# Kernel optimization log

Hardware: AMD Instinct MI355X
Metric: run time of the kernel (lower is better)

## Reference

```python
import jax, jax.numpy as jnp
import numpy as np

AGENT_RADIUS = 0.5
SAFETY_DIST = 0.1
QP_ITERS = 300


def _qp_solve(p, G, h):
    """Batched QP: min_u 0.5 u^T u + p^T u  s.t.  G u <= h  (Q = I).
    Solved in the dual by projected gradient ascent (differentiable, fixed iters).
    p: [B,2], G: [B,m,2], h: [B,m] -> u: [B,2]
    """
    GGt = jnp.einsum('bmi,bni->bmn', G, G)                 # [B,m,m]
    q = jnp.einsum('bmi,bi->bm', G, p) + h                 # [B,m]
    # Lipschitz upper bound per sample (Frobenius norm of GG^T)
    L = jnp.sqrt(jnp.sum(GGt * GGt, axis=(1, 2))) + 1e-6   # [B]
    alpha = (1.0 / L)[:, None]

    def step(lam, _):
        grad = jnp.einsum('bmn,bn->bm', GGt, lam) + q
        lam = jnp.maximum(lam - alpha * grad, 0.0)
        return lam, None

    lam0 = jnp.zeros_like(h)
    lam, _ = jax.lax.scan(step, lam0, None, length=QP_ITERS)
    u = -p - jnp.einsum('bmi,bm->bi', G, lam)
    return u


def setup_inputs() -> dict:
    key = jax.random.key(0)
    ks = jax.random.split(key, 20)
    B, F, H1, H2 = 8192, 8, 1024, 512

    def w(k, i, o):
        return (jax.random.normal(k, (i, o), jnp.float32) / np.sqrt(i)).astype(jnp.float32)

    obs_xy = jax.random.uniform(ks[17], (8, 2), jnp.float32, -10.0, 10.0)
    obs_r = jax.random.uniform(ks[18], (8, 1), jnp.float32, 0.3, 0.8)
    return {
        'x': jax.random.normal(ks[0], (B, F), jnp.float32),
        'mean': 0.1 * jax.random.normal(ks[1], (F,), jnp.float32),
        'std': jax.random.uniform(ks[2], (F,), jnp.float32, 0.5, 1.5),
        'W1': w(ks[3], F, H1), 'b1': jnp.zeros((H1,), jnp.float32),
        'W21': w(ks[4], H1, H2), 'b21': jnp.zeros((H2,), jnp.float32),
        'W22': w(ks[5], H1, H2), 'b22': jnp.zeros((H2,), jnp.float32),
        'W23': w(ks[6], H1, H2), 'b23': jnp.zeros((H2,), jnp.float32),
        'W31': w(ks[7], H2, 2), 'b31': jnp.zeros((2,), jnp.float32),
        'W32': w(ks[8], H2, 2), 'b32': jnp.zeros((2,), jnp.float32),
        'W33': w(ks[9], H2, 1), 'b33': jnp.zeros((1,), jnp.float32),
        'obstacles': jnp.concatenate([obs_xy, obs_r], axis=1),  # [8,3] (x,y,r)
        'sgn': 1,
    }


def reference(x, mean, std, W1, b1, W21, b21, W22, b22, W23, b23,
              W31, b31, W32, b32, W33, b33, obstacles, sgn):
    B = x.shape[0]
    x0 = x * std + mean                                   # un-normalized state [B,8]

    h1 = jax.nn.relu(x @ W1 + b1)
    x21 = jax.nn.relu(h1 @ W21 + b21)
    x22 = jax.nn.relu(h1 @ W22 + b22)
    x23 = jax.nn.relu(h1 @ W23 + b23)
    x31 = x21 @ W31 + b31                                 # QP linear term p [B,2]
    x32 = 4.0 * jax.nn.sigmoid(x22 @ W32 + b32)           # CBF gains p1,p2 [B,2]
    x33 = 4.0 * jax.nn.sigmoid(x23 @ W33 + b33)           # liveness gain (unused, smg off)

    px, py, theta, v = x0[:, 0], x0[:, 1], x0[:, 2], x0[:, 3]
    st, ct = jnp.sin(theta)[:, None], jnp.cos(theta)[:, None]
    vb = v[:, None]

    # static obstacles broadcast to batch + opponent as last obstacle -> [B, m]
    ox = jnp.concatenate([jnp.broadcast_to(obstacles[:, 0][None], (B, obstacles.shape[0])), x0[:, 4:5]], axis=1)
    oy = jnp.concatenate([jnp.broadcast_to(obstacles[:, 1][None], (B, obstacles.shape[0])), x0[:, 5:6]], axis=1)
    orad = jnp.concatenate([jnp.broadcast_to(obstacles[:, 2][None], (B, obstacles.shape[0])),
                            jnp.full((B, 1), AGENT_RADIUS, x0.dtype)], axis=1)

    R = AGENT_RADIUS + orad + SAFETY_DIST
    dx = px[:, None] - ox                                  # [B,m]
    dy = py[:, None] - oy

    barrier = dx * dx + dy * dy - R * R
    barrier_dot = 2.0 * dx * vb * ct + 2.0 * dy * vb * st
    Lf2b = (2.0 * v * v)[:, None]
    LgLfbu1 = -2.0 * dx * vb * st + 2.0 * dy * vb * ct
    LgLfbu2 = 2.0 * dx * ct + 2.0 * dy * st
    G = jnp.stack([-LgLfbu1, -LgLfbu2], axis=-1)           # [B,m,2]
    p1, p2 = x32[:, 0:1], x32[:, 1:2]
    h = Lf2b + (p1 + p2) * barrier_dot + p1 * p2 * barrier # [B,m]

    u = _qp_solve(x31, G, h)                               # [B,2]
    return u
```

## Files before the change

### kernel.cpp

```cpp
#include <hip/hip_runtime.h>
#include <cstdint>
#include <cstddef>

typedef unsigned short u16;
typedef u16   u16x8  __attribute__((ext_vector_type(8)));
typedef u16   u16x4  __attribute__((ext_vector_type(4)));
typedef __bf16 bf16x8 __attribute__((ext_vector_type(8)));
typedef float f32x4  __attribute__((ext_vector_type(4)));
typedef float f32x2  __attribute__((ext_vector_type(2)));

__device__ __forceinline__ float bf2f(u16 v) {
  unsigned int u = ((unsigned int)v) << 16;
  return __builtin_bit_cast(float, u);
}
__device__ __forceinline__ u16 f2bf(float f) {
  unsigned int x = __builtin_bit_cast(unsigned int, f);
  x += 0x7fffu + ((x >> 16) & 1u);
  return (u16)(x >> 16);
}

__global__ __launch_bounds__(256) void k_prep(const float* __restrict__ W21,
                                              const float* __restrict__ W22,
                                              u16* __restrict__ Wt,
                                              const float* __restrict__ x,
                                              const float* __restrict__ W1,
                                              const float* __restrict__ b1,
                                              u16* __restrict__ h1,
                                              float* __restrict__ head) {
  __shared__ u16 s[64][65];
  const int b = blockIdx.x;
  if (b < 256) {
    const int mat = b >> 7;
    const int tt  = b & 127;
    const int k0  = (tt >> 3) * 64;
    const int n0  = (tt & 7) * 64;
    const float* W = mat ? W22 : W21;
    const int tx = threadIdx.x & 63;
    const int ty = threadIdx.x >> 6;
#pragma unroll
    for (int i = 0; i < 16; ++i) {
      int r = i * 4 + ty;
      s[r][tx] = f2bf(W[(size_t)(k0 + r) * 512 + n0 + tx]);
    }
    __syncthreads();
    const int nbase = mat * 512 + n0;
#pragma unroll
    for (int i = 0; i < 16; ++i) {
      int r = i * 4 + ty;
      Wt[(size_t)(nbase + r) * 1024 + k0 + tx] = s[tx][r];
    }
  } else {
    const int row = b - 256;
    if (threadIdx.x == 0)
      *(f32x4*)(head + 4 * (size_t)row) = f32x4{0.f, 0.f, 0.f, 0.f};
    const int c4 = threadIdx.x * 4;
    const float* xr = x + (size_t)row * 8;
    f32x4 acc = *(const f32x4*)(b1 + c4);
#pragma unroll
    for (int f = 0; f < 8; ++f) {
      float xv = xr[f];
      f32x4 wv = *(const f32x4*)(W1 + f * 1024 + c4);
#pragma unroll
      for (int e = 0; e < 4; ++e) acc[e] = fmaf(xv, wv[e], acc[e]);
    }
    u16x4 o;
#pragma unroll
    for (int e = 0; e < 4; ++e) o[e] = f2bf(fmaxf(acc[e], 0.f));
    *(u16x4*)(h1 + (size_t)row * 1024 + c4) = o;
  }
}

__global__ __launch_bounds__(256) void k_gemm(const u16* __restrict__ A,
                                              const u16* __restrict__ Bt,
                                              const float* __restrict__ b21,
                                              const float* __restrict__ b22,
                                              const float* __restrict__ W31,
                                              const float* __restrict__ W32,
                                              float* __restrict__ head) {
  constexpr int K  = 1024;
  constexpr int BK = 32;
  constexpr int NT = K / BK;
  __shared__ u16 As[2][128 * BK];
  __shared__ u16 Bs[2][128 * BK];

  const int t    = threadIdx.x;
  const int row0 = blockIdx.y * 128;
  const int col0 = blockIdx.x * 128;
  const int w    = t >> 6;
  const int lane = t & 63;
  const int wr   = w >> 1, wc = w & 1;
  const int lrow = lane & 15;
  const int lk   = (lane >> 4) * 8;

  const int c0 = t, c1 = 256 + t;
  const u16* gA0 = A  + (size_t)(row0 + (c0 >> 2)) * K + (c0 & 3) * 8;
  const u16* gA1 = A  + (size_t)(row0 + (c1 >> 2)) * K + (c1 & 3) * 8;
  const u16* gB0 = Bt + (size_t)(col0 + (c0 >> 2)) * K + (c0 & 3) * 8;
  const u16* gB1 = Bt + (size_t)(col0 + (c1 >> 2)) * K + (c1 & 3) * 8;
  const int lo0 = c0 * 8, lo1 = c1 * 8;

  f32x4 acc[4][4];
#pragma unroll
  for (int i = 0; i < 4; ++i)
#pragma unroll
    for (int j = 0; j < 4; ++j) acc[i][j] = f32x4{0.f, 0.f, 0.f, 0.f};

  {
    u16x8 ta0 = *(const u16x8*)gA0;
    u16x8 ta1 = *(const u16x8*)gA1;
    u16x8 tb0 = *(const u16x8*)gB0;
    u16x8 tb1 = *(const u16x8*)gB1;
    *(u16x8*)(As[0] + lo0) = ta0;
    *(u16x8*)(As[0] + lo1) = ta1;
    *(u16x8*)(Bs[0] + lo0) = tb0;
    *(u16x8*)(Bs[0] + lo1) = tb1;
  }
  u16x8 na0 = *(const u16x8*)(gA0 + BK);
  u16x8 na1 = *(const u16x8*)(gA1 + BK);
  u16x8 nb0 = *(const u16x8*)(gB0 + BK);
  u16x8 nb1 = *(const u16x8*)(gB1 + BK);

  for (int kt = 0; kt < NT; ++kt) {
    const int cur = kt & 1, nxt = cur ^ 1;
    __syncthreads();

    const int koff = (kt + 2 < NT ? kt + 2 : NT - 1) * BK;
    u16x8 fa0 = *(const u16x8*)(gA0 + koff);
    u16x8 fa1 = *(const u16x8*)(gA1 + koff);
    u16x8 fb0 = *(const u16x8*)(gB0 + koff);
    u16x8 fb1 = *(const u16x8*)(gB1 + koff);

    bf16x8 af[4], bfr[4];
#pragma unroll
    for (int i = 0; i < 4; ++i)
      af[i] = __builtin_bit_cast(bf16x8,
          *(const u16x8*)(As[cur] + (wr * 64 + i * 16 + lrow) * BK + lk));
#pragma unroll
    for (int j = 0; j < 4; ++j)
      bfr[j] = __builtin_bit_cast(bf16x8,
          *(const u16x8*)(Bs[cur] + (wc * 64 + j * 16 + lrow) * BK + lk));
#pragma unroll
    for (int i = 0; i < 4; ++i)
#pragma unroll
      for (int j = 0; j < 4; ++j)
        acc[i][j] = __builtin_amdgcn_mfma_f32_16x16x32_bf16(af[i], bfr[j], acc[i][j], 0, 0, 0);

    if (kt + 1 < NT) {
      *(u16x8*)(As[nxt] + lo0) = na0;
      *(u16x8*)(As[nxt] + lo1) = na1;
      *(u16x8*)(Bs[nxt] + lo0) = nb0;
      *(u16x8*)(Bs[nxt] + lo1) = nb1;
    }
    na0 = fa0; na1 = fa1; nb0 = fb0; nb1 = fb1;
  }

  const bool isX21 = (col0 < 512);
  const float* Wh  = isX21 ? W31 : W32;
  const int   hoff = isX21 ? 0 : 2;

  float hx[16], hy[16];
#pragma unroll
  for (int n = 0; n < 16; ++n) { hx[n] = 0.f; hy[n] = 0.f; }
#pragma unroll
  for (int j = 0; j < 4; ++j) {
    int col  = col0 + wc * 64 + j * 16 + lrow;
    int wcol = col & 511;
    f32x2 wv = *(const f32x2*)(Wh + 2 * wcol);
    float bias = isX21 ? b21[col] : b22[wcol];
#pragma unroll
    for (int i = 0; i < 4; ++i)
#pragma unroll
      for (int rr = 0; rr < 4; ++rr) {
        float v = fmaxf(acc[i][j][rr] + bias, 0.f);
        hx[i * 4 + rr] = fmaf(v, wv[0], hx[i * 4 + rr]);
        hy[i * 4 + rr] = fmaf(v, wv[1], hy[i * 4 + rr]);
      }
  }
#pragma unroll
  for (int m = 1; m <= 8; m <<= 1) {
#pragma unroll
    for (int n = 0; n < 16; ++n) {
      hx[n] += __shfl_xor(hx[n], m, 64);
      hy[n] += __shfl_xor(hy[n], m, 64);
    }
  }
  if (lrow == 0) {
    const int rq = (lane >> 4) * 4;
#pragma unroll
    for (int i = 0; i < 4; ++i)
#pragma unroll
      for (int rr = 0; rr < 4; ++rr) {
        int row = row0 + wr * 64 + i * 16 + rq + rr;
        atomicAdd(head + 4 * (size_t)row + hoff,     hx[i * 4 + rr]);
        atomicAdd(head + 4 * (size_t)row + hoff + 1, hy[i * 4 + rr]);
      }
  }
}

__global__ __launch_bounds__(256) void k_qp(const float* __restrict__ x,
                                            const float* __restrict__ mean_,
                                            const float* __restrict__ std_,
                                            const float* __restrict__ head,
                                            const float* __restrict__ b31,
                                            const float* __restrict__ b32,
                                            const float* __restrict__ obstacles,
                                            float* __restrict__ out) {
  const int r = blockIdx.x * 256 + threadIdx.x;
  f32x4 hd = *(const f32x4*)(head + 4 * (size_t)r);
  float p0  = hd[0] + b31[0];
  float p1v = hd[1] + b31[1];
  float pp1 = 4.f / (1.f + expf(-(hd[2] + b32[0])));
  float pp2 = 4.f / (1.f + expf(-(hd[3] + b32[1])));

  const f32x4* xp = (const f32x4*)(x + (size_t)r * 8);
  f32x4 xa = xp[0], xb = xp[1];
  float px = xa[0] * std_[0] + mean_[0];
  float py = xa[1] * std_[1] + mean_[1];
  float th = xa[2] * std_[2] + mean_[2];
  float v  = xa[3] * std_[3] + mean_[3];
  float ax = xb[0] * std_[4] + mean_[4];
  float ay = xb[1] * std_[5] + mean_[5];
  float st = sinf(th), ct = cosf(th);
  float Lf2b = 2.f * v * v;

  float G0[9], G1[9], q[9];
  float s00 = 0.f, s01 = 0.f, s11 = 0.f;
#pragma unroll
  for (int m = 0; m < 9; ++m) {
    float ox, oy, orad;
    if (m < 8) {
      ox = obstacles[m * 3]; oy = obstacles[m * 3 + 1]; orad = obstacles[m * 3 + 2];
    } else { ox = ax; oy = ay; orad = 0.5f; }
    float R  = 0.6f + orad;
    float dx = px - ox, dy = py - oy;
    float bar  = dx * dx + dy * dy - R * R;
    float dct  = dx * ct + dy * st;
    float bdot = 2.f * v * dct;
    float g0 = 2.f * v * (dx * st - dy * ct);
    float g1 = -2.f * dct;
    float h  = Lf2b + (pp1 + pp2) * bdot + pp1 * pp2 * bar;
    G0[m] = g0; G1[m] = g1;
    q[m] = g0 * p0 + g1 * p1v + h;
    s00 += g0 * g0; s01 += g0 * g1; s11 += g1 * g1;
  }
  float L = sqrtf(s00 * s00 + 2.f * s01 * s01 + s11 * s11) + 1e-6f;
  float alpha = 1.f / L;

  float lam[9];
#pragma unroll
  for (int m = 0; m < 9; ++m) lam[m] = 0.f;
  for (int it = 0; it < 300; ++it) {
    float pr0[9], pr1[9];
#pragma unroll
    for (int m = 0; m < 9; ++m) { pr0[m] = G0[m] * lam[m]; pr1[m] = G1[m] * lam[m]; }
    float t0 = (((pr0[0] + pr0[1]) + (pr0[2] + pr0[3])) +
                ((pr0[4] + pr0[5]) + (pr0[6] + pr0[7]))) + pr0[8];
    float t1 = (((pr1[0] + pr1[1]) + (pr1[2] + pr1[3])) +
                ((pr1[4] + pr1[5]) + (pr1[6] + pr1[7]))) + pr1[8];
#pragma unroll
    for (int m = 0; m < 9; ++m) {
      float g = fmaf(G0[m], t0, fmaf(G1[m], t1, q[m]));
      lam[m] = fmaxf(fmaf(-alpha, g, lam[m]), 0.f);
    }
  }
  float u0 = -p0, u1 = -p1v;
#pragma unroll
  for (int m = 0; m < 9; ++m) { u0 = fmaf(-G0[m], lam[m], u0); u1 = fmaf(-G1[m], lam[m], u1); }
  *(f32x2*)(out + 2 * (size_t)r) = f32x2{u0, u1};
}

extern "C" void kernel_launch(void* const* d_in, const int* in_sizes, int n_in,
                              void* d_out, int out_size, void* d_ws, size_t ws_size,
                              hipStream_t stream) {
  const float* x    = (const float*)d_in[0];
  const float* mean_= (const float*)d_in[1];
  const float* std_ = (const float*)d_in[2];
  const float* W1   = (const float*)d_in[3];
  const float* b1   = (const float*)d_in[4];
  const float* W21  = (const float*)d_in[5];
  const float* b21  = (const float*)d_in[6];
  const float* W22  = (const float*)d_in[7];
  const float* b22  = (const float*)d_in[8];
  const float* W31  = (const float*)d_in[11];
  const float* b31  = (const float*)d_in[12];
  const float* W32  = (const float*)d_in[13];
  const float* b32  = (const float*)d_in[14];
  const float* obst = (const float*)d_in[17];
  float* out = (float*)d_out;

  char* ws = (char*)d_ws;
  u16*   Wt   = (u16*)ws;
  u16*   h1   = (u16*)(ws + (size_t)(1 << 21));
  float* head = (float*)(ws + (size_t)(1 << 21) + (size_t)(1 << 24));

  k_prep<<<256 + 8192, 256, 0, stream>>>(W21, W22, Wt, x, W1, b1, h1, head);
  k_gemm<<<dim3(8, 64), 256, 0, stream>>>(h1, Wt, b21, b22, W31, W32, head);
  k_qp  <<<32, 256, 0, stream>>>(x, mean_, std_, head, b31, b32, obst, out);
}
```

Before: 171.6 us.

## Retile head GEMM to 64x64 blocks with 32x32 MFMA and padded LDS

```diff
diff --git a/kernel.cpp b/kernel.cpp
--- a/kernel.cpp
+++ b/kernel.cpp
@@ -8,6 +8,7 @@
 typedef __bf16 bf16x8 __attribute__((ext_vector_type(8)));
 typedef float f32x4  __attribute__((ext_vector_type(4)));
 typedef float f32x2  __attribute__((ext_vector_type(2)));
+typedef float f32x16 __attribute__((ext_vector_type(16)));
 
 __device__ __forceinline__ float bf2f(u16 v) {
   unsigned int u = ((unsigned int)v) << 16;
@@ -50,27 +51,35 @@
       Wt[(size_t)(nbase + r) * 1024 + k0 + tx] = s[tx][r];
     }
   } else {
-    const int row = b - 256;
-    if (threadIdx.x == 0)
-      *(f32x4*)(head + 4 * (size_t)row) = f32x4{0.f, 0.f, 0.f, 0.f};
+    const int row0 = (b - 256) * 8;
+    if (threadIdx.x < 8)
+      *(f32x4*)(head + 4 * (size_t)(row0 + threadIdx.x)) = f32x4{0.f, 0.f, 0.f, 0.f};
     const int c4 = threadIdx.x * 4;
-    const float* xr = x + (size_t)row * 8;
-    f32x4 acc = *(const f32x4*)(b1 + c4);
+    f32x4 bv = *(const f32x4*)(b1 + c4);
+    f32x4 acc[8];
+#pragma unroll
+    for (int r = 0; r < 8; ++r) acc[r] = bv;
 #pragma unroll
     for (int f = 0; f < 8; ++f) {
-      float xv = xr[f];
       f32x4 wv = *(const f32x4*)(W1 + f * 1024 + c4);
 #pragma unroll
-      for (int e = 0; e < 4; ++e) acc[e] = fmaf(xv, wv[e], acc[e]);
-    }
-    u16x4 o;
-#pragma unroll
-    for (int e = 0; e < 4; ++e) o[e] = f2bf(fmaxf(acc[e], 0.f));
-    *(u16x4*)(h1 + (size_t)row * 1024 + c4) = o;
-  }
-}
-
-__global__ __launch_bounds__(256) void k_gemm(const u16* __restrict__ A,
+      for (int r = 0; r < 8; ++r) {
+        float xv = x[(size_t)(row0 + r) * 8 + f];
+#pragma unroll
+        for (int e = 0; e < 4; ++e) acc[r][e] = fmaf(xv, wv[e], acc[r][e]);
+      }
+    }
+#pragma unroll
+    for (int r = 0; r < 8; ++r) {
+      u16x4 o;
+#pragma unroll
+      for (int e = 0; e < 4; ++e) o[e] = f2bf(fmaxf(acc[r][e], 0.f));
+      *(u16x4*)(h1 + (size_t)(row0 + r) * 1024 + c4) = o;
+    }
+  }
+}
+
+__global__ __launch_bounds__(128) void k_gemm(const u16* __restrict__ A,
                                               const u16* __restrict__ Bt,
                                               const float* __restrict__ b21,
                                               const float* __restrict__ b22,
@@ -80,120 +89,97 @@
   constexpr int K  = 1024;
   constexpr int BK = 32;
   constexpr int NT = K / BK;
-  __shared__ u16 As[2][128 * BK];
-  __shared__ u16 Bs[2][128 * BK];
+  constexpr int ST = 40;
+  __shared__ u16 As[64 * ST];
+  __shared__ u16 Bs[64 * ST];
 
   const int t    = threadIdx.x;
-  const int row0 = blockIdx.y * 128;
-  const int col0 = blockIdx.x * 128;
+  const int col0 = blockIdx.x * 64;
+  const int row0 = blockIdx.y * 64;
   const int w    = t >> 6;
   const int lane = t & 63;
-  const int wr   = w >> 1, wc = w & 1;
-  const int lrow = lane & 15;
-  const int lk   = (lane >> 4) * 8;
-
-  const int c0 = t, c1 = 256 + t;
+  const int ln   = lane & 31;
+  const int kh   = lane >> 5;
+
+  const int c0 = t, c1 = 128 + t;
   const u16* gA0 = A  + (size_t)(row0 + (c0 >> 2)) * K + (c0 & 3) * 8;
   const u16* gA1 = A  + (size_t)(row0 + (c1 >> 2)) * K + (c1 & 3) * 8;
   const u16* gB0 = Bt + (size_t)(col0 + (c0 >> 2)) * K + (c0 & 3) * 8;
   const u16* gB1 = Bt + (size_t)(col0 + (c1 >> 2)) * K + (c1 & 3) * 8;
-  const int lo0 = c0 * 8, lo1 = c1 * 8;
-
-  f32x4 acc[4][4];
-#pragma unroll
-  for (int i = 0; i < 4; ++i)
-#pragma unroll
-    for (int j = 0; j < 4; ++j) acc[i][j] = f32x4{0.f, 0.f, 0.f, 0.f};
-
-  {
-    u16x8 ta0 = *(const u16x8*)gA0;
-    u16x8 ta1 = *(const u16x8*)gA1;
-    u16x8 tb0 = *(const u16x8*)gB0;
-    u16x8 tb1 = *(const u16x8*)gB1;
-    *(u16x8*)(As[0] + lo0) = ta0;
-    *(u16x8*)(As[0] + lo1) = ta1;
-    *(u16x8*)(Bs[0] + lo0) = tb0;
-    *(u16x8*)(Bs[0] + lo1) = tb1;
-  }
-  u16x8 na0 = *(const u16x8*)(gA0 + BK);
-  u16x8 na1 = *(const u16x8*)(gA1 + BK);
-  u16x8 nb0 = *(const u16x8*)(gB0 + BK);
-  u16x8 nb1 = *(const u16x8*)(gB1 + BK);
+  const int lA0 = (c0 >> 2) * ST + (c0 & 3) * 8;
+  const int lA1 = (c1 >> 2) * ST + (c1 & 3) * 8;
+
+  f32x16 acc0, acc1;
+#pragma unroll
+  for (int e = 0; e < 16; ++e) { acc0[e] = 0.f; acc1[e] = 0.f; }
+
+  u16x8 ra0 = *(const u16x8*)gA0;
+  u16x8 ra1 = *(const u16x8*)gA1;
+  u16x8 rb0 = *(const u16x8*)gB0;
+  u16x8 rb1 = *(const u16x8*)gB1;
 
   for (int kt = 0; kt < NT; ++kt) {
-    const int cur = kt & 1, nxt = cur ^ 1;
     __syncthreads();
-
-    const int koff = (kt + 2 < NT ? kt + 2 : NT - 1) * BK;
-    u16x8 fa0 = *(const u16x8*)(gA0 + koff);
-    u16x8 fa1 = *(const u16x8*)(gA1 + koff);
-    u16x8 fb0 = *(const u16x8*)(gB0 + koff);
-    u16x8 fb1 = *(const u16x8*)(gB1 + koff);
-
-    bf16x8 af[4], bfr[4];
-#pragma unroll
-    for (int i = 0; i < 4; ++i)
-      af[i] = __builtin_bit_cast(bf16x8,
-          *(const u16x8*)(As[cur] + (wr * 64 + i * 16 + lrow) * BK + lk));
-#pragma unroll
-    for (int j = 0; j < 4; ++j)
-      bfr[j] = __builtin_bit_cast(bf16x8,
-          *(const u16x8*)(Bs[cur] + (wc * 64 + j * 16 + lrow) * BK + lk));
-#pragma unroll
-    for (int i = 0; i < 4; ++i)
-#pragma unroll
-      for (int j = 0; j < 4; ++j)
-        acc[i][j] = __builtin_amdgcn_mfma_f32_16x16x32_bf16(af[i], bfr[j], acc[i][j], 0, 0, 0);
-
+    *(u16x8*)(As + lA0) = ra0;
+    *(u16x8*)(As + lA1) = ra1;
+    *(u16x8*)(Bs + lA0) = rb0;
+    *(u16x8*)(Bs + lA1) = rb1;
     if (kt + 1 < NT) {
-      *(u16x8*)(As[nxt] + lo0) = na0;
-      *(u16x8*)(As[nxt] + lo1) = na1;
-      *(u16x8*)(Bs[nxt] + lo0) = nb0;
-      *(u16x8*)(Bs[nxt] + lo1) = nb1;
-    }
-    na0 = fa0; na1 = fa1; nb0 = fb0; nb1 = fb1;
-  }
-
-  const bool isX21 = (col0 < 512);
-  const float* Wh  = isX21 ? W31 : W32;
-  const int   hoff = isX21 ? 0 : 2;
-
-  float hx[16], hy[16];
-#pragma unroll
-  for (int n = 0; n < 16; ++n) { hx[n] = 0.f; hy[n] = 0.f; }
-#pragma unroll
-  for (int j = 0; j < 4; ++j) {
-    int col  = col0 + wc * 64 + j * 16 + lrow;
-    int wcol = col & 511;
-    f32x2 wv = *(const f32x2*)(Wh + 2 * wcol);
-    float bias = isX21 ? b21[col] : b22[wcol];
-#pragma unroll
-    for (int i = 0; i < 4; ++i)
-#pragma unroll
-      for (int rr = 0; rr < 4; ++rr) {
-        float v = fmaxf(acc[i][j][rr] + bias, 0.f);
-        hx[i * 4 + rr] = fmaf(v, wv[0], hx[i * 4 + rr]);
-        hy[i * 4 + rr] = fmaf(v, wv[1], hy[i * 4 + rr]);
+      const int ko = (kt + 1) * BK;
+      ra0 = *(const u16x8*)(gA0 + ko);
+      ra1 = *(const u16x8*)(gA1 + ko);
+      rb0 = *(const u16x8*)(gB0 + ko);
+      rb1 = *(const u16x8*)(gB1 + ko);
+    }
+    __syncthreads();
+
+    bf16x8 a0s0 = __builtin_bit_cast(bf16x8, *(const u16x8*)(As + (ln)      * ST +      kh * 8));
+    bf16x8 a1s0 = __builtin_bit_cast(bf16x8, *(const u16x8*)(As + (32 + ln) * ST +      kh * 8));
+    bf16x8 b_s0 = __builtin_bit_cast(bf16x8, *(const u16x8*)(Bs + (w * 32 + ln) * ST +  kh * 8));
+    bf16x8 a0s1 = __builtin_bit_cast(bf16x8, *(const u16x8*)(As + (ln)      * ST + 16 + kh * 8));
+    bf16x8 a1s1 = __builtin_bit_cast(bf16x8, *(const u16x8*)(As + (32 + ln) * ST + 16 + kh * 8));
+    bf16x8 b_s1 = __builtin_bit_cast(bf16x8, *(const u16x8*)(Bs + (w * 32 + ln) * ST + 16 + kh * 8));
+
+    acc0 = __builtin_amdgcn_mfma_f32_32x32x16_bf16(a0s0, b_s0, acc0, 0, 0, 0);
+    acc1 = __builtin_amdgcn_mfma_f32_32x32x16_bf16(a1s0, b_s0, acc1, 0, 0, 0);
+    acc0 = __builtin_amdgcn_mfma_f32_32x32x16_bf16(a0s1, b_s1, acc0, 0, 0, 0);
+    acc1 = __builtin_amdgcn_mfma_f32_32x32x16_bf16(a1s1, b_s1, acc1, 0, 0, 0);
+  }
+
+  const int col   = col0 + w * 32 + ln;
+  const bool isX21 = (col < 512);
+  const float* Wh = isX21 ? W31 : W32;
+  const int  hoff = isX21 ? 0 : 2;
+  const int  wcol = col & 511;
+  f32x2 wv = *(const f32x2*)(Wh + 2 * wcol);
+  const float bias = isX21 ? b21[col] : b22[wcol];
+
+#pragma unroll
+  for (int i = 0; i < 2; ++i) {
+    f32x16 a = i ? acc1 : acc0;
+    float hx[16], hy[16];
+#pragma unroll
+    for (int r = 0; r < 16; ++r) {
+      float v = fmaxf(a[r] + bias, 0.f);
+      hx[r] = v * wv[0];
+      hy[r] = v * wv[1];
+    }
+#pragma unroll
+    for (int m = 1; m <= 16; m <<= 1) {
+#pragma unroll
+      for (int r = 0; r < 16; ++r) {
+        hx[r] += __shfl_xor(hx[r], m, 64);
+        hy[r] += __shfl_xor(hy[r], m, 64);
       }
-  }
-#pragma unroll
-  for (int m = 1; m <= 8; m <<= 1) {
-#pragma unroll
-    for (int n = 0; n < 16; ++n) {
-      hx[n] += __shfl_xor(hx[n], m, 64);
-      hy[n] += __shfl_xor(hy[n], m, 64);
-    }
-  }
-  if (lrow == 0) {
-    const int rq = (lane >> 4) * 4;
-#pragma unroll
-    for (int i = 0; i < 4; ++i)
-#pragma unroll
-      for (int rr = 0; rr < 4; ++rr) {
-        int row = row0 + wr * 64 + i * 16 + rq + rr;
-        atomicAdd(head + 4 * (size_t)row + hoff,     hx[i * 4 + rr]);
-        atomicAdd(head + 4 * (size_t)row + hoff + 1, hy[i * 4 + rr]);
+    }
+    if (ln == 0) {
+#pragma unroll
+      for (int r = 0; r < 16; ++r) {
+        int grow = row0 + i * 32 + (r & 3) + 8 * (r >> 2) + 4 * kh;
+        atomicAdd(head + 4 * (size_t)grow + hoff,     hx[r]);
+        atomicAdd(head + 4 * (size_t)grow + hoff + 1, hy[r]);
       }
+    }
   }
 }
 
@@ -293,7 +279,7 @@
   u16*   h1   = (u16*)(ws + (size_t)(1 << 21));
   float* head = (float*)(ws + (size_t)(1 << 21) + (size_t)(1 << 24));
 
-  k_prep<<<256 + 8192, 256, 0, stream>>>(W21, W22, Wt, x, W1, b1, h1, head);
-  k_gemm<<<dim3(8, 64), 256, 0, stream>>>(h1, Wt, b21, b22, W31, W32, head);
+  k_prep<<<256 + 1024, 256, 0, stream>>>(W21, W22, Wt, x, W1, b1, h1, head);
+  k_gemm<<<dim3(16, 128), 128, 0, stream>>>(h1, Wt, b21, b22, W31, W32, head);
   k_qp  <<<32, 256, 0, stream>>>(x, mean_, std_, head, b31, b32, obst, out);
 }
```

Measured after the change: 206.8 us. +20.5%, slower.

## Use direct global-to-LDS loads with XOR swizzle and batch layer-1 rows per block

Applied to the files above, without the earlier changes.

```diff
diff --git a/kernel.cpp b/kernel.cpp
--- a/kernel.cpp
+++ b/kernel.cpp
@@ -17,6 +17,12 @@
   unsigned int x = __builtin_bit_cast(unsigned int, f);
   x += 0x7fffu + ((x >> 16) & 1u);
   return (u16)(x >> 16);
+}
+
+__device__ __forceinline__ void gld_lds16(const u16* g, u16* l) {
+  __builtin_amdgcn_global_load_lds(
+      (const __attribute__((address_space(1))) unsigned int*)g,
+      (__attribute__((address_space(3))) unsigned int*)l, 16, 0, 0);
 }
 
 __global__ __launch_bounds__(256) void k_prep(const float* __restrict__ W21,
@@ -50,23 +56,31 @@
       Wt[(size_t)(nbase + r) * 1024 + k0 + tx] = s[tx][r];
     }
   } else {
-    const int row = b - 256;
-    if (threadIdx.x == 0)
-      *(f32x4*)(head + 4 * (size_t)row) = f32x4{0.f, 0.f, 0.f, 0.f};
+    const int row0 = (b - 256) * 8;
+    if (threadIdx.x < 8)
+      *(f32x4*)(head + 4 * (size_t)(row0 + threadIdx.x)) = f32x4{0.f, 0.f, 0.f, 0.f};
     const int c4 = threadIdx.x * 4;
-    const float* xr = x + (size_t)row * 8;
-    f32x4 acc = *(const f32x4*)(b1 + c4);
+    f32x4 bv = *(const f32x4*)(b1 + c4);
+    f32x4 acc[8];
+#pragma unroll
+    for (int r = 0; r < 8; ++r) acc[r] = bv;
 #pragma unroll
     for (int f = 0; f < 8; ++f) {
-      float xv = xr[f];
       f32x4 wv = *(const f32x4*)(W1 + f * 1024 + c4);
 #pragma unroll
-      for (int e = 0; e < 4; ++e) acc[e] = fmaf(xv, wv[e], acc[e]);
-    }
-    u16x4 o;
-#pragma unroll
-    for (int e = 0; e < 4; ++e) o[e] = f2bf(fmaxf(acc[e], 0.f));
-    *(u16x4*)(h1 + (size_t)row * 1024 + c4) = o;
+      for (int r = 0; r < 8; ++r) {
+        float xv = x[(size_t)(row0 + r) * 8 + f];
+#pragma unroll
+        for (int e = 0; e < 4; ++e) acc[r][e] = fmaf(xv, wv[e], acc[r][e]);
+      }
+    }
+#pragma unroll
+    for (int r = 0; r < 8; ++r) {
+      u16x4 o;
+#pragma unroll
+      for (int e = 0; e < 4; ++e) o[e] = f2bf(fmaxf(acc[r][e], 0.f));
+      *(u16x4*)(h1 + (size_t)(row0 + r) * 1024 + c4) = o;
+    }
   }
 }
 
@@ -80,24 +94,28 @@
   constexpr int K  = 1024;
   constexpr int BK = 32;
   constexpr int NT = K / BK;
-  __shared__ u16 As[2][128 * BK];
-  __shared__ u16 Bs[2][128 * BK];
+  __shared__ u16 As[2][128 * 32];
+  __shared__ u16 Bs[2][128 * 32];
 
   const int t    = threadIdx.x;
-  const int row0 = blockIdx.y * 128;
-  const int col0 = blockIdx.x * 128;
+  const int row0 = blockIdx.x * 128;
+  const int col0 = blockIdx.y * 128;
   const int w    = t >> 6;
   const int lane = t & 63;
   const int wr   = w >> 1, wc = w & 1;
   const int lrow = lane & 15;
-  const int lk   = (lane >> 4) * 8;
-
-  const int c0 = t, c1 = 256 + t;
-  const u16* gA0 = A  + (size_t)(row0 + (c0 >> 2)) * K + (c0 & 3) * 8;
-  const u16* gA1 = A  + (size_t)(row0 + (c1 >> 2)) * K + (c1 & 3) * 8;
-  const u16* gB0 = Bt + (size_t)(col0 + (c0 >> 2)) * K + (c0 & 3) * 8;
-  const u16* gB1 = Bt + (size_t)(col0 + (c1 >> 2)) * K + (c1 & 3) * 8;
-  const int lo0 = c0 * 8, lo1 = c1 * 8;
+  const int kq   = lane >> 4;
+
+  const int s0 = t, s1 = 256 + t;
+  const int g0c = (s0 & 3) ^ ((s0 >> 3) & 3);
+  const int g1c = (s1 & 3) ^ ((s1 >> 3) & 3);
+  const u16* gA0 = A  + (size_t)(row0 + (s0 >> 2)) * K + g0c * 8;
+  const u16* gA1 = A  + (size_t)(row0 + (s1 >> 2)) * K + g1c * 8;
+  const u16* gB0 = Bt + (size_t)(col0 + (s0 >> 2)) * K + g0c * 8;
+  const u16* gB1 = Bt + (size_t)(col0 + (s1 >> 2)) * K + g1c * 8;
+  const int lo0 = s0 * 8, lo1 = s1 * 8;
+
+  const int pc = kq ^ ((lrow >> 1) & 3);
 
   f32x4 acc[4][4];
 #pragma unroll
@@ -105,53 +123,37 @@
 #pragma unroll
     for (int j = 0; j < 4; ++j) acc[i][j] = f32x4{0.f, 0.f, 0.f, 0.f};
 
-  {
-    u16x8 ta0 = *(const u16x8*)gA0;
-    u16x8 ta1 = *(const u16x8*)gA1;
-    u16x8 tb0 = *(const u16x8*)gB0;
-    u16x8 tb1 = *(const u16x8*)gB1;
-    *(u16x8*)(As[0] + lo0) = ta0;
-    *(u16x8*)(As[0] + lo1) = ta1;
-    *(u16x8*)(Bs[0] + lo0) = tb0;
-    *(u16x8*)(Bs[0] + lo1) = tb1;
-  }
-  u16x8 na0 = *(const u16x8*)(gA0 + BK);
-  u16x8 na1 = *(const u16x8*)(gA1 + BK);
-  u16x8 nb0 = *(const u16x8*)(gB0 + BK);
-  u16x8 nb1 = *(const u16x8*)(gB1 + BK);
+  gld_lds16(gA0, As[0] + lo0);
+  gld_lds16(gA1, As[0] + lo1);
+  gld_lds16(gB0, Bs[0] + lo0);
+  gld_lds16(gB1, Bs[0] + lo1);
 
   for (int kt = 0; kt < NT; ++kt) {
     const int cur = kt & 1, nxt = cur ^ 1;
     __syncthreads();
 
-    const int koff = (kt + 2 < NT ? kt + 2 : NT - 1) * BK;
-    u16x8 fa0 = *(const u16x8*)(gA0 + koff);
-    u16x8 fa1 = *(const u16x8*)(gA1 + koff);
-    u16x8 fb0 = *(const u16x8*)(gB0 + koff);
-    u16x8 fb1 = *(const u16x8*)(gB1 + koff);
+    if (kt + 1 < NT) {
+      const int ko = (kt + 1) * BK;
+      gld_lds16(gA0 + ko, As[nxt] + lo0);
+      gld_lds16(gA1 + ko, As[nxt] + lo1);
+      gld_lds16(gB0 + ko, Bs[nxt] + lo0);
+      gld_lds16(gB1 + ko, Bs[nxt] + lo1);
+    }
 
     bf16x8 af[4], bfr[4];
 #pragma unroll
     for (int i = 0; i < 4; ++i)
       af[i] = __builtin_bit_cast(bf16x8,
-          *(const u16x8*)(As[cur] + (wr * 64 + i * 16 + lrow) * BK + lk));
+          *(const u16x8*)(As[cur] + (wr * 64 + i * 16 + lrow) * 32 + pc * 8));
 #pragma unroll
     for (int j = 0; j < 4; ++j)
       bfr[j] = __builtin_bit_cast(bf16x8,
-          *(const u16x8*)(Bs[cur] + (wc * 64 + j * 16 + lrow) * BK + lk));
+          *(const u16x8*)(Bs[cur] + (wc * 64 + j * 16 + lrow) * 32 + pc * 8));
 #pragma unroll
     for (int i = 0; i < 4; ++i)
 #pragma unroll
       for (int j = 0; j < 4; ++j)
         acc[i][j] = __builtin_amdgcn_mfma_f32_16x16x32_bf16(af[i], bfr[j], acc[i][j], 0, 0, 0);
-
-    if (kt + 1 < NT) {
-      *(u16x8*)(As[nxt] + lo0) = na0;
-      *(u16x8*)(As[nxt] + lo1) = na1;
-      *(u16x8*)(Bs[nxt] + lo0) = nb0;
-      *(u16x8*)(Bs[nxt] + lo1) = nb1;
-    }
-    na0 = fa0; na1 = fa1; nb0 = fb0; nb1 = fb1;
   }
 
   const bool isX21 = (col0 < 512);
@@ -185,12 +187,11 @@
     }
   }
   if (lrow == 0) {
-    const int rq = (lane >> 4) * 4;
 #pragma unroll
     for (int i = 0; i < 4; ++i)
 #pragma unroll
       for (int rr = 0; rr < 4; ++rr) {
-        int row = row0 + wr * 64 + i * 16 + rq + rr;
+        int row = row0 + wr * 64 + i * 16 + kq * 4 + rr;
         atomicAdd(head + 4 * (size_t)row + hoff,     hx[i * 4 + rr]);
         atomicAdd(head + 4 * (size_t)row + hoff + 1, hy[i * 4 + rr]);
       }
@@ -293,7 +294,7 @@
   u16*   h1   = (u16*)(ws + (size_t)(1 << 21));
   float* head = (float*)(ws + (size_t)(1 << 21) + (size_t)(1 << 24));
 
-  k_prep<<<256 + 8192, 256, 0, stream>>>(W21, W22, Wt, x, W1, b1, h1, head);
-  k_gemm<<<dim3(8, 64), 256, 0, stream>>>(h1, Wt, b21, b22, W31, W32, head);
+  k_prep<<<256 + 1024, 256, 0, stream>>>(W21, W22, Wt, x, W1, b1, h1, head);
+  k_gemm<<<dim3(64, 8), 256, 0, stream>>>(h1, Wt, b21, b22, W31, W32, head);
   k_qp  <<<32, 256, 0, stream>>>(x, mean_, std_, head, b31, b32, obst, out);
 }
```

New measurement: 173.7 us. About the same (+1.2%).
